# Kernel optimization log

Measured on AMD Instinct MI355X. Metric: run time of the kernel, lower is better.

The kernel has to match this reference:

```python
import jax, jax.numpy as jnp
import numpy as np

N_NODES = 100000

def gcn_conv(x, edge_index, W, b):
    # GCNConv with normalize=True and self-loops:
    # out = D^{-1/2} (A + I) D^{-1/2} (x W) + b
    h = x @ W                                   # [N, out]
    src, dst = edge_index[0], edge_index[1]
    deg = jax.ops.segment_sum(jnp.ones(src.shape[0], h.dtype), dst,
                              num_segments=N_NODES) + 1.0  # +1 for self loop
    dinv = jax.lax.rsqrt(deg)
    norm = dinv[src] * dinv[dst]                # [E]
    agg = jax.ops.segment_sum(h[src] * norm[:, None], dst,
                              num_segments=N_NODES)        # [N, out]
    agg = agg + h * (1.0 / deg)[:, None]        # self-loop term: norm_ii = 1/deg_i
    return agg + b


def setup_inputs() -> dict:
    key = jax.random.key(0)
    k0, k1, k2, k3 = jax.random.split(key, 4)
    N, E, F_IN, H, C = N_NODES, 1600000, 256, 128, 40
    x = jax.random.normal(k0, (N, F_IN), dtype=jnp.float32)
    edge_index = jax.random.randint(k1, (2, E), 0, N, dtype=jnp.int64)
    W1 = jax.random.normal(k2, (F_IN, H), dtype=jnp.float32) * (1.0 / np.sqrt(F_IN))
    b1 = jnp.zeros((H,), jnp.float32)
    W2 = jax.random.normal(k3, (H, C), dtype=jnp.float32) * (1.0 / np.sqrt(H))
    b2 = jnp.zeros((C,), jnp.float32)
    return {"x": x, "edge_index": edge_index, "W1": W1, "b1": b1, "W2": W2, "b2": b2}


def reference(x, edge_index, W1, b1, W2, b2):
    # layer 1 + ReLU (dropout = identity in eval mode)
    h = jax.nn.relu(gcn_conv(x, edge_index, W1, b1))
    # final layer (no activation)
    return gcn_conv(h, edge_index, W2, b2)
```

## Files before the change

kernel.cpp:

```cpp
#include <hip/hip_runtime.h>
#include <hip/hip_bf16.h>


#define FIN 256
#define HDIM 128
#define CDIM 40
#define CAP 8192
#define EC 8192

typedef __attribute__((ext_vector_type(8))) short bf16x8;
typedef __attribute__((ext_vector_type(4))) float f32x4;
typedef __attribute__((ext_vector_type(2))) float f32x2;

__device__ inline short f2bf(float f) {
    unsigned u = __float_as_uint(f);
    unsigned r = (u + 0x7FFFu + ((u >> 16) & 1u)) >> 16;
    return (short)r;
}
__device__ inline float bflo(unsigned u) { return __uint_as_float(u << 16); }
__device__ inline float bfhi(unsigned u) { return __uint_as_float(u & 0xFFFF0000u); }
__device__ inline f32x2 unpk(unsigned u) { return (f32x2){bflo(u), bfhi(u)}; }
__device__ inline float ub0(unsigned u) { return (float)(u & 255u); }
__device__ inline float ub1(unsigned u) { return (float)((u >> 8) & 255u); }
__device__ inline float ub2(unsigned u) { return (float)((u >> 16) & 255u); }
__device__ inline float ub3(unsigned u) { return (float)(u >> 24); }

__global__ __launch_bounds__(1024) void scatter_k(const int* __restrict__ ei, int* __restrict__ gcnt,
                                                  int* __restrict__ bmem, int E, int NBUCK) {
    __shared__ int hist[512];
    __shared__ int base[512];
    const int tid = threadIdx.x;
    for (int t = tid; t < NBUCK; t += 1024) hist[t] = 0;
    __syncthreads();
    const int e0 = blockIdx.x * EC;
    const int e1 = min(E, e0 + EC);
    for (int e = e0 + tid; e < e1; e += 1024) atomicAdd(&hist[ei[E + e] >> 8], 1);
    __syncthreads();
    for (int t = tid; t < NBUCK; t += 1024) base[t] = atomicAdd(&gcnt[t], hist[t]);
    __syncthreads();
    for (int e = e0 + tid; e < e1; e += 1024) {
        int s = ei[e];
        int d = ei[E + e];
        int b = d >> 8;
        int pos = atomicAdd(&base[b], 1);
        bmem[b * CAP + pos] = s | ((d & 255) << 20);
    }
}

__global__ __launch_bounds__(256) void p2_build_k(const int* __restrict__ bmem, const int* __restrict__ bcnt,
                                                  int* __restrict__ csr, int2* __restrict__ nseg,
                                                  float* __restrict__ dinv, float* __restrict__ invd,
                                                  const float* __restrict__ W1, const float* __restrict__ W2,
                                                  short* __restrict__ W1T, short* __restrict__ W2T, int N) {
    __shared__ int hist[256], cur[256], sc[256];
    __shared__ int stage[CAP];
    const int b = blockIdx.x;
    const int tid = threadIdx.x;

    for (int idx = b * 256 + tid; idx < FIN * HDIM + 48 * HDIM; idx += gridDim.x * 256) {
        if (idx < FIN * HDIM) {
            int k = idx >> 7, n = idx & 127;
            W1T[n * FIN + k] = f2bf(W1[idx]);
        } else {
            int j = idx - FIN * HDIM;
            int c = j >> 7, k = j & 127;
            W2T[j] = (c < CDIM) ? f2bf(W2[k * CDIM + c]) : (short)0;
        }
    }

    int cnt = bcnt[b];
    if (cnt > CAP) cnt = CAP;
    const int* src = bmem + b * CAP;
    hist[tid] = 0;
    __syncthreads();
    for (int j = tid; j < cnt; j += 256) atomicAdd(&hist[src[j] >> 20], 1);
    __syncthreads();
    int v = hist[tid];
    sc[tid] = v;
    __syncthreads();
    for (int off = 1; off < 256; off <<= 1) {
        int t = (tid >= off) ? sc[tid - off] : 0;
        __syncthreads();
        sc[tid] += t;
        __syncthreads();
    }
    int excl = sc[tid] - v;
    cur[tid] = excl;
    int i = b * 256 + tid;
    if (i < N) {
        nseg[i] = make_int2(b * CAP + excl, v);
        float dg = (float)(v + 1);
        dinv[i] = rsqrtf(dg);
        invd[i] = 1.0f / dg;
    }
    __syncthreads();
    for (int j = tid; j < cnt; j += 256) {
        int rec = src[j];
        int pos = atomicAdd(&cur[rec >> 20], 1);
        stage[pos] = rec & 0xFFFFF;
    }
    __syncthreads();
    int* dst = csr + b * CAP;
    for (int j = tid; j < cnt; j += 256) dst[j] = stage[j];
}

#define LDSTRIDE 40
__global__ __launch_bounds__(256) void gemm1_mfma_k(const float* __restrict__ X,
                                                    const short* __restrict__ W1T,
                                                    const float* __restrict__ dinv,
                                                    unsigned char* __restrict__ T1q,
                                                    float* __restrict__ scl,
                                                    float* __restrict__ wsc, int N) {
    __shared__ short SH[128 * LDSTRIDE * 2];
    short* As = SH;
    short* Bs = SH + 128 * LDSTRIDE;
    const int tid = threadIdx.x;
    const int lane = tid & 63;
    const int wid = tid >> 6;
    const int w0 = wid & 1, w1 = wid >> 1;
    const int quad = lane >> 4;
    const int l16 = lane & 15;
    const int rowbase = blockIdx.x * 128;
    const int sr = tid >> 1;
    const int sh = tid & 1;

    f32x4 acc[4][4];
#pragma unroll
    for (int a = 0; a < 4; a++)
#pragma unroll
        for (int b = 0; b < 4; b++) acc[a][b] = (f32x4){0.f, 0.f, 0.f, 0.f};

    const int arow = min(rowbase + sr, N - 1);
    const float* xsrc = X + (size_t)arow * FIN + sh * 16;
    const int4* bsrc = (const int4*)(W1T + (size_t)sr * FIN + sh * 16);

    for (int k0 = 0; k0 < FIN; k0 += 32) {
        float vals[16];
        *(float4*)&vals[0]  = *(const float4*)(xsrc + k0);
        *(float4*)&vals[4]  = *(const float4*)(xsrc + k0 + 4);
        *(float4*)&vals[8]  = *(const float4*)(xsrc + k0 + 8);
        *(float4*)&vals[12] = *(const float4*)(xsrc + k0 + 12);
        short tmp[16];
#pragma unroll
        for (int c = 0; c < 16; c++) tmp[c] = f2bf(vals[c]);
        ((int4*)&As[sr * LDSTRIDE + sh * 16])[0] = ((int4*)tmp)[0];
        ((int4*)&As[sr * LDSTRIDE + sh * 16])[1] = ((int4*)tmp)[1];
        int4 b0 = bsrc[k0 >> 3];
        int4 b1 = bsrc[(k0 >> 3) + 1];
        ((int4*)&Bs[sr * LDSTRIDE + sh * 16])[0] = b0;
        ((int4*)&Bs[sr * LDSTRIDE + sh * 16])[1] = b1;
        __syncthreads();

        bf16x8 afr[4], bfr[4];
#pragma unroll
        for (int mt = 0; mt < 4; mt++)
            afr[mt] = *(const bf16x8*)&As[(w1 * 64 + mt * 16 + l16) * LDSTRIDE + quad * 8];
#pragma unroll
        for (int nt = 0; nt < 4; nt++)
            bfr[nt] = *(const bf16x8*)&Bs[(w0 * 64 + nt * 16 + l16) * LDSTRIDE + quad * 8];
#pragma unroll
        for (int mt = 0; mt < 4; mt++)
#pragma unroll
            for (int nt = 0; nt < 4; nt++)
                acc[mt][nt] = __builtin_amdgcn_mfma_f32_16x16x32_bf16(afr[mt], bfr[nt], acc[mt][nt], 0, 0, 0);
        __syncthreads();
    }

    unsigned char* qbuf = (unsigned char*)SH;
    float* rmaxb = (float*)((char*)SH + 16384);
#pragma unroll
    for (int mt = 0; mt < 4; mt++) {
#pragma unroll
        for (int r = 0; r < 4; r++) {
            float m = fabsf(acc[mt][0][r]);
            m = fmaxf(m, fabsf(acc[mt][1][r]));
            m = fmaxf(m, fabsf(acc[mt][2][r]));
            m = fmaxf(m, fabsf(acc[mt][3][r]));
#pragma unroll
            for (int off = 1; off < 16; off <<= 1) m = fmaxf(m, __shfl_xor(m, off));
            rmaxb[w0 * 128 + w1 * 64 + mt * 16 + quad * 4 + r] = m;
        }
    }
    __syncthreads();
    if (tid < 128) {
        int grow = rowbase + tid;
        if (grow < N) {
            float rv = fmaxf(rmaxb[tid], rmaxb[128 + tid]);
            float s = rv * (1.f / 127.f);
            scl[grow] = s;
            wsc[grow] = s * dinv[grow];
        }
    }
#pragma unroll
    for (int mt = 0; mt < 4; mt++) {
#pragma unroll
        for (int r = 0; r < 4; r++) {
            const int row = w1 * 64 + mt * 16 + quad * 4 + r;
            float rv = fmaxf(rmaxb[row], rmaxb[128 + row]);
            float qinv = rv > 0.f ? 127.f / rv : 0.f;
#pragma unroll
            for (int nt = 0; nt < 4; nt++) {
                int qi = (int)rintf(acc[mt][nt][r] * qinv) + 128;
                qi = qi < 0 ? 0 : (qi > 255 ? 255 : qi);
                qbuf[row * 128 + w0 * 64 + nt * 16 + l16] = (unsigned char)qi;
            }
        }
    }
    __syncthreads();
#pragma unroll
    for (int it = 0; it < 4; it++) {
        int idx = tid + it * 256;
        int row = idx >> 3;
        if (rowbase + row < N)
            ((uint4*)(T1q + (size_t)(rowbase + row) * 128))[idx & 7] = ((const uint4*)qbuf)[idx];
    }
}

__global__ __launch_bounds__(256) void agg1_k(const unsigned char* __restrict__ T1q, const int2* __restrict__ nseg,
                                              const int* __restrict__ csr, const float* __restrict__ wsc,
                                              const float* __restrict__ scl, const float* __restrict__ dinv,
                                              const float* __restrict__ invd, const float* __restrict__ b1,
                                              unsigned* __restrict__ Hb, int N) {
    const int lane = threadIdx.x & 63;
    const int quad = lane >> 4;
    const int ql = lane & 15;
    const int i = blockIdx.x * 4 + (threadIdx.x >> 6);
    if (i >= N) return;
    const int2 sg = nseg[i];
    const int e0 = sg.x, deg = sg.y;
    int sv = 0; float wv = 0.f;
    if (lane < deg) { sv = csr[e0 + lane]; wv = wsc[sv]; }

    const uint2* rowp = (const uint2*)T1q;
    uint2 us = rowp[i * 16 + ql];
    const float sscale = scl[i];

    f32x2 acc[4]; float asum = 0.f;
#pragma unroll
    for (int t = 0; t < 4; t++) acc[t] = (f32x2){0.f, 0.f};

    const int dmain = deg < 64 ? deg : 64;
    for (int j = 0; j < dmain; j += 16) {
        const int i0 = j + quad, i1 = j + 4 + quad, i2 = j + 8 + quad, i3 = j + 12 + quad;
        int s0 = __shfl(sv, i0); int s1 = __shfl(sv, i1);
        int s2 = __shfl(sv, i2); int s3 = __shfl(sv, i3);
        float w0 = __shfl(wv, i0); float w1 = __shfl(wv, i1);
        float w2 = __shfl(wv, i2); float w3 = __shfl(wv, i3);
        w0 = (i0 < dmain) ? w0 : 0.f;
        w1 = (i1 < dmain) ? w1 : 0.f;
        w2 = (i2 < dmain) ? w2 : 0.f;
        w3 = (i3 < dmain) ? w3 : 0.f;
        uint2 u0 = rowp[s0 * 16 + ql];
        uint2 u1 = rowp[s1 * 16 + ql];
        uint2 u2 = rowp[s2 * 16 + ql];
        uint2 u3 = rowp[s3 * 16 + ql];
        asum += w0 + w1 + w2 + w3;
        f32x2 W0 = (f32x2){w0, w0}, W1v = (f32x2){w1, w1}, W2v = (f32x2){w2, w2}, W3v = (f32x2){w3, w3};
        acc[0] += W0 * (f32x2){ub0(u0.x), ub1(u0.x)} + W1v * (f32x2){ub0(u1.x), ub1(u1.x)}
                + W2v * (f32x2){ub0(u2.x), ub1(u2.x)} + W3v * (f32x2){ub0(u3.x), ub1(u3.x)};
        acc[1] += W0 * (f32x2){ub2(u0.x), ub3(u0.x)} + W1v * (f32x2){ub2(u1.x), ub3(u1.x)}
                + W2v * (f32x2){ub2(u2.x), ub3(u2.x)} + W3v * (f32x2){ub2(u3.x), ub3(u3.x)};
        acc[2] += W0 * (f32x2){ub0(u0.y), ub1(u0.y)} + W1v * (f32x2){ub0(u1.y), ub1(u1.y)}
                + W2v * (f32x2){ub0(u2.y), ub1(u2.y)} + W3v * (f32x2){ub0(u3.y), ub1(u3.y)};
        acc[3] += W0 * (f32x2){ub2(u0.y), ub3(u0.y)} + W1v * (f32x2){ub2(u1.y), ub3(u1.y)}
                + W2v * (f32x2){ub2(u2.y), ub3(u2.y)} + W3v * (f32x2){ub2(u3.y), ub3(u3.y)};
    }
    const int eEnd = e0 + deg;
    for (int e = e0 + 64; e < eEnd; e += 4) {
        int idx = e + quad;
        int cl = idx < eEnd ? idx : eEnd - 1;
        int sj = csr[cl];
        float wj = (idx < eEnd) ? wsc[sj] : 0.f;
        uint2 u = rowp[sj * 16 + ql];
        asum += wj;
        f32x2 Wj = (f32x2){wj, wj};
        acc[0] += Wj * (f32x2){ub0(u.x), ub1(u.x)};
        acc[1] += Wj * (f32x2){ub2(u.x), ub3(u.x)};
        acc[2] += Wj * (f32x2){ub0(u.y), ub1(u.y)};
        acc[3] += Wj * (f32x2){ub2(u.y), ub3(u.y)};
    }
#pragma unroll
    for (int t = 0; t < 4; t++) {
        acc[t].x += __shfl_xor(acc[t].x, 16); acc[t].y += __shfl_xor(acc[t].y, 16);
        acc[t].x += __shfl_xor(acc[t].x, 32); acc[t].y += __shfl_xor(acc[t].y, 32);
    }
    asum += __shfl_xor(asum, 16);
    asum += __shfl_xor(asum, 32);

    const float di = dinv[i];
    const float sf2 = invd[i] * sscale;
    const float K = -128.f * (sf2 + di * asum);
    float4 bA = *(const float4*)(b1 + ql * 8);
    float4 bB = *(const float4*)(b1 + ql * 8 + 4);
    float o0 = fmaxf(bA.x + sf2 * ub0(us.x) + di * acc[0].x + K, 0.f);
    float o1 = fmaxf(bA.y + sf2 * ub1(us.x) + di * acc[0].y + K, 0.f);
    float o2 = fmaxf(bA.z + sf2 * ub2(us.x) + di * acc[1].x + K, 0.f);
    float o3 = fmaxf(bA.w + sf2 * ub3(us.x) + di * acc[1].y + K, 0.f);
    float o4 = fmaxf(bB.x + sf2 * ub0(us.y) + di * acc[2].x + K, 0.f);
    float o5 = fmaxf(bB.y + sf2 * ub1(us.y) + di * acc[2].y + K, 0.f);
    float o6 = fmaxf(bB.z + sf2 * ub2(us.y) + di * acc[3].x + K, 0.f);
    float o7 = fmaxf(bB.w + sf2 * ub3(us.y) + di * acc[3].y + K, 0.f);
    uint4 pk;
    pk.x = ((unsigned)(unsigned short)f2bf(o0)) | (((unsigned)(unsigned short)f2bf(o1)) << 16);
    pk.y = ((unsigned)(unsigned short)f2bf(o2)) | (((unsigned)(unsigned short)f2bf(o3)) << 16);
    pk.z = ((unsigned)(unsigned short)f2bf(o4)) | (((unsigned)(unsigned short)f2bf(o5)) << 16);
    pk.w = ((unsigned)(unsigned short)f2bf(o6)) | (((unsigned)(unsigned short)f2bf(o7)) << 16);
    if (quad == 0) ((uint4*)(Hb + (size_t)i * 64))[ql] = pk;
}

__global__ __launch_bounds__(256) void gemm2_mfma_k(const short* __restrict__ Hb,
                                                    const short* __restrict__ W2T,
                                                    short* __restrict__ T2b, int N) {
    __shared__ short As[128 * LDSTRIDE];
    __shared__ short Bs[48 * LDSTRIDE];
    const int tid = threadIdx.x;
    const int lane = tid & 63;
    const int wid = tid >> 6;
    const int quad = lane >> 4;
    const int l16 = lane & 15;
    const int rowbase = blockIdx.x * 128;
    const int sr = tid >> 1;
    const int sh = tid & 1;

    f32x4 acc[2][3];
#pragma unroll
    for (int a = 0; a < 2; a++)
#pragma unroll
        for (int b = 0; b < 3; b++) acc[a][b] = (f32x4){0.f, 0.f, 0.f, 0.f};

    const int arow = min(rowbase + sr, N - 1);
    const int4* asrc = (const int4*)(Hb + (size_t)arow * HDIM + sh * 16);
    const int br = tid >> 1, bh = tid & 1;
    const int4* bsrc = (const int4*)(W2T + br * HDIM + bh * 16);

    for (int k0 = 0; k0 < HDIM; k0 += 32) {
        int4 a0 = asrc[k0 >> 3];
        int4 a1 = asrc[(k0 >> 3) + 1];
        ((int4*)&As[sr * LDSTRIDE + sh * 16])[0] = a0;
        ((int4*)&As[sr * LDSTRIDE + sh * 16])[1] = a1;
        if (tid < 96) {
            int4 b0 = bsrc[k0 >> 3];
            int4 b1 = bsrc[(k0 >> 3) + 1];
            ((int4*)&Bs[br * LDSTRIDE + bh * 16])[0] = b0;
            ((int4*)&Bs[br * LDSTRIDE + bh * 16])[1] = b1;
        }
        __syncthreads();
        bf16x8 afr[2], bfr[3];
#pragma unroll
        for (int mt = 0; mt < 2; mt++)
            afr[mt] = *(const bf16x8*)&As[(wid * 32 + mt * 16 + l16) * LDSTRIDE + quad * 8];
#pragma unroll
        for (int nt = 0; nt < 3; nt++)
            bfr[nt] = *(const bf16x8*)&Bs[(nt * 16 + l16) * LDSTRIDE + quad * 8];
#pragma unroll
        for (int mt = 0; mt < 2; mt++)
#pragma unroll
            for (int nt = 0; nt < 3; nt++)
                acc[mt][nt] = __builtin_amdgcn_mfma_f32_16x16x32_bf16(afr[mt], bfr[nt], acc[mt][nt], 0, 0, 0);
        __syncthreads();
    }
#pragma unroll
    for (int mt = 0; mt < 2; mt++) {
#pragma unroll
        for (int r = 0; r < 4; r++) {
            int row = rowbase + wid * 32 + mt * 16 + quad * 4 + r;
            if (row < N) {
#pragma unroll
                for (int nt = 0; nt < 3; nt++) {
                    int col = nt * 16 + l16;
                    T2b[(size_t)row * 48 + col] = f2bf(acc[mt][nt][r]);
                }
            }
        }
    }
}

__global__ __launch_bounds__(256) void agg2_k(const short* __restrict__ T2b, const int2* __restrict__ nseg,
                                              const int* __restrict__ csr, const float* __restrict__ dinv,
                                              const float* __restrict__ invd, const float* __restrict__ b2,
                                              float* __restrict__ OUT, int N) {
    const int lane = threadIdx.x & 63;
    const int oct = lane >> 3;
    const int olr = lane & 7;
    const int ol = olr < 6 ? olr : 5;
    const bool act = olr < 6;
    const int i = blockIdx.x * 4 + (threadIdx.x >> 6);
    if (i >= N) return;
    const int2 sg = nseg[i];
    const int e0 = sg.x, deg = sg.y;
    int sv = 0; float wv = 0.f;
    if (lane < deg) { sv = csr[e0 + lane]; wv = dinv[sv]; }

    const uint4* rowp = (const uint4*)T2b;
    f32x2 acc[4];
#pragma unroll
    for (int t = 0; t < 4; t++) acc[t] = (f32x2){0.f, 0.f};

    const int dmain = deg < 64 ? deg : 64;
    for (int j = 0; j < dmain; j += 16) {
        const int i0 = j + oct, i1 = j + 8 + oct;
        int s0 = __shfl(sv, i0); int s1 = __shfl(sv, i1);
        float w0 = __shfl(wv, i0); float w1 = __shfl(wv, i1);
        w0 = (i0 < dmain && act) ? w0 : 0.f;
        w1 = (i1 < dmain && act) ? w1 : 0.f;
        uint4 u0 = rowp[s0 * 6 + ol];
        uint4 u1 = rowp[s1 * 6 + ol];
        f32x2 W0 = (f32x2){w0, w0}, W1v = (f32x2){w1, w1};
        acc[0] += W0 * unpk(u0.x) + W1v * unpk(u1.x);
        acc[1] += W0 * unpk(u0.y) + W1v * unpk(u1.y);
        acc[2] += W0 * unpk(u0.z) + W1v * unpk(u1.z);
        acc[3] += W0 * unpk(u0.w) + W1v * unpk(u1.w);
    }
    const int eEnd = e0 + deg;
    for (int e = e0 + 64; e < eEnd; e += 8) {
        int idx = e + oct;
        int cl = idx < eEnd ? idx : eEnd - 1;
        int sj = csr[cl];
        float wj = (idx < eEnd && act) ? dinv[sj] : 0.f;
        uint4 u = rowp[sj * 6 + ol];
        f32x2 Wj = (f32x2){wj, wj};
        acc[0] += Wj * unpk(u.x);
        acc[1] += Wj * unpk(u.y);
        acc[2] += Wj * unpk(u.z);
        acc[3] += Wj * unpk(u.w);
    }
#pragma unroll
    for (int t = 0; t < 4; t++) {
        acc[t].x += __shfl_xor(acc[t].x, 8);  acc[t].y += __shfl_xor(acc[t].y, 8);
        acc[t].x += __shfl_xor(acc[t].x, 16); acc[t].y += __shfl_xor(acc[t].y, 16);
        acc[t].x += __shfl_xor(acc[t].x, 32); acc[t].y += __shfl_xor(acc[t].y, 32);
    }
    if (oct == 0 && olr < 5) {
        const float di = dinv[i], sf = invd[i];
        uint4 us = rowp[i * 6 + olr];
        float4 bA = *(const float4*)(b2 + olr * 8);
        float4 bB = *(const float4*)(b2 + olr * 8 + 4);
        float4 oA, oB;
        oA.x = bA.x + sf * bflo(us.x) + di * acc[0].x;
        oA.y = bA.y + sf * bfhi(us.x) + di * acc[0].y;
        oA.z = bA.z + sf * bflo(us.y) + di * acc[1].x;
        oA.w = bA.w + sf * bfhi(us.y) + di * acc[1].y;
        oB.x = bB.x + sf * bflo(us.z) + di * acc[2].x;
        oB.y = bB.y + sf * bfhi(us.z) + di * acc[2].y;
        oB.z = bB.z + sf * bflo(us.w) + di * acc[3].x;
        oB.w = bB.w + sf * bfhi(us.w) + di * acc[3].y;
        *(float4*)(OUT + (size_t)i * CDIM + olr * 8) = oA;
        *(float4*)(OUT + (size_t)i * CDIM + olr * 8 + 4) = oB;
    }
}

extern "C" void kernel_launch(void* const* d_in, const int* in_sizes, int n_in,
                              void* d_out, int out_size, void* d_ws, size_t ws_size,
                              hipStream_t stream) {
    const float* x   = (const float*)d_in[0];
    const int*   ei  = (const int*)d_in[1];
    const float* W1  = (const float*)d_in[2];
    const float* b1  = (const float*)d_in[3];
    const float* W2  = (const float*)d_in[4];
    const float* b2  = (const float*)d_in[5];
    float*       out = (float*)d_out;

    const int Hd  = in_sizes[3];
    const int Fin = in_sizes[2] / Hd;
    const int N   = in_sizes[0] / Fin;
    const int E   = in_sizes[1] / 2;

    const int NBUCK = (N + 255) / 256;
    const int NB1   = (E + EC - 1) / EC;

    char* base = (char*)d_ws;
    size_t off = 0;
    auto alloc = [&](size_t bytes) -> void* {
        void* p = base + off;
        off += (bytes + 255) & ~(size_t)255;
        return p;
    };
    size_t bmemB = (size_t)NBUCK * CAP * 4;
    size_t t1qB  = (size_t)N * 128;
    size_t regA  = bmemB > t1qB ? bmemB : t1qB;
    char* pA = (char*)alloc(regA);
    int*           bmem = (int*)pA;
    unsigned char* t1q  = (unsigned char*)pA;

    int*      gcnt = (int*)alloc((size_t)NBUCK * 4);
    int*      csr  = (int*)alloc((size_t)NBUCK * CAP * 4);
    int2*     nseg = (int2*)alloc((size_t)N * 8);
    float*    dinv = (float*)alloc((size_t)N * 4);
    float*    invd = (float*)alloc((size_t)N * 4);
    float*    scl  = (float*)alloc((size_t)N * 4);
    float*    wsc  = (float*)alloc((size_t)N * 4);
    short*    W1T  = (short*)alloc((size_t)HDIM * FIN * 2);
    short*    W2T  = (short*)alloc((size_t)48 * HDIM * 2);
    unsigned* hb   = (unsigned*)alloc((size_t)N * HDIM * 2);
    short*    t2b  = (short*)alloc((size_t)N * 48 * 2);

    hipMemsetAsync(gcnt, 0, (size_t)NBUCK * 4, stream);
    scatter_k<<<NB1, 1024, 0, stream>>>(ei, gcnt, bmem, E, NBUCK);
    p2_build_k<<<NBUCK, 256, 0, stream>>>(bmem, gcnt, csr, nseg, dinv, invd, W1, W2, W1T, W2T, N);

    gemm1_mfma_k<<<(N + 127) / 128, 256, 0, stream>>>(x, W1T, dinv, t1q, scl, wsc, N);
    agg1_k<<<(N + 3) / 4, 256, 0, stream>>>(t1q, nseg, csr, wsc, scl, dinv, invd, b1, hb, N);
    gemm2_mfma_k<<<(N + 127) / 128, 256, 0, stream>>>((const short*)hb, W2T, t2b, N);
    agg2_k<<<(N + 3) / 4, 256, 0, stream>>>(t2b, nseg, csr, dinv, invd, b2, out, N);
}
```

Measured before the change: 321.7 us.

## Fuse second GEMM into layer-1 aggregation and quantize layer-2 features to uint8

The layer-1 aggregation kernel now multiplies each node's ReLU output by W2 with per-wave MFMA, using lane shuffles to build the A fragment. It then quantizes the 40-wide result to uint8 with a per-row scale and writes 64-byte rows. This drops the bf16 hidden buffer, the separate gemm2 kernel launch and its global round trip. The second aggregation gathers uint8 rows (64 B instead of 96 B per neighbor) and applies the same zero-point correction used in layer 1. Running the MFMA on a single row per wave leaves most of each tile idle, and 8-bit quantization of the layer-2 features adds rounding error to the output.

```diff
diff --git a/kernel.cpp b/kernel.cpp
--- a/kernel.cpp
+++ b/kernel.cpp
@@ -220,7 +220,10 @@
                                               const int* __restrict__ csr, const float* __restrict__ wsc,
                                               const float* __restrict__ scl, const float* __restrict__ dinv,
                                               const float* __restrict__ invd, const float* __restrict__ b1,
-                                              unsigned* __restrict__ Hb, int N) {
+                                              const short* __restrict__ W2T,
+                                              unsigned char* __restrict__ T2q,
+                                              float* __restrict__ scl2, float* __restrict__ wsc2, int N) {
+    __shared__ unsigned char qs[4][64];
     const int lane = threadIdx.x & 63;
     const int quad = lane >> 4;
     const int ql = lane & 15;
@@ -305,94 +308,67 @@
     pk.y = ((unsigned)(unsigned short)f2bf(o2)) | (((unsigned)(unsigned short)f2bf(o3)) << 16);
     pk.z = ((unsigned)(unsigned short)f2bf(o4)) | (((unsigned)(unsigned short)f2bf(o5)) << 16);
     pk.w = ((unsigned)(unsigned short)f2bf(o6)) | (((unsigned)(unsigned short)f2bf(o7)) << 16);
-    if (quad == 0) ((uint4*)(Hb + (size_t)i * 64))[ql] = pk;
-}
-
-__global__ __launch_bounds__(256) void gemm2_mfma_k(const short* __restrict__ Hb,
-                                                    const short* __restrict__ W2T,
-                                                    short* __restrict__ T2b, int N) {
-    __shared__ short As[128 * LDSTRIDE];
-    __shared__ short Bs[48 * LDSTRIDE];
-    const int tid = threadIdx.x;
-    const int lane = tid & 63;
-    const int wid = tid >> 6;
-    const int quad = lane >> 4;
-    const int l16 = lane & 15;
-    const int rowbase = blockIdx.x * 128;
-    const int sr = tid >> 1;
-    const int sh = tid & 1;
-
-    f32x4 acc[2][3];
-#pragma unroll
-    for (int a = 0; a < 2; a++)
-#pragma unroll
-        for (int b = 0; b < 3; b++) acc[a][b] = (f32x4){0.f, 0.f, 0.f, 0.f};
-
-    const int arow = min(rowbase + sr, N - 1);
-    const int4* asrc = (const int4*)(Hb + (size_t)arow * HDIM + sh * 16);
-    const int br = tid >> 1, bh = tid & 1;
-    const int4* bsrc = (const int4*)(W2T + br * HDIM + bh * 16);
-
-    for (int k0 = 0; k0 < HDIM; k0 += 32) {
-        int4 a0 = asrc[k0 >> 3];
-        int4 a1 = asrc[(k0 >> 3) + 1];
-        ((int4*)&As[sr * LDSTRIDE + sh * 16])[0] = a0;
-        ((int4*)&As[sr * LDSTRIDE + sh * 16])[1] = a1;
-        if (tid < 96) {
-            int4 b0 = bsrc[k0 >> 3];
-            int4 b1 = bsrc[(k0 >> 3) + 1];
-            ((int4*)&Bs[br * LDSTRIDE + bh * 16])[0] = b0;
-            ((int4*)&Bs[br * LDSTRIDE + bh * 16])[1] = b1;
-        }
-        __syncthreads();
-        bf16x8 afr[2], bfr[3];
-#pragma unroll
-        for (int mt = 0; mt < 2; mt++)
-            afr[mt] = *(const bf16x8*)&As[(wid * 32 + mt * 16 + l16) * LDSTRIDE + quad * 8];
+
+    const bf16x8* w2p = (const bf16x8*)W2T;
+    f32x4 acc2[3];
+#pragma unroll
+    for (int nt = 0; nt < 3; nt++) acc2[nt] = (f32x4){0.f, 0.f, 0.f, 0.f};
+#pragma unroll
+    for (int kf = 0; kf < 4; kf++) {
+        const int srcl = kf * 4 + quad;
+        bf16x8 af;
+        ((int*)&af)[0] = __shfl((int)pk.x, srcl);
+        ((int*)&af)[1] = __shfl((int)pk.y, srcl);
+        ((int*)&af)[2] = __shfl((int)pk.z, srcl);
+        ((int*)&af)[3] = __shfl((int)pk.w, srcl);
 #pragma unroll
         for (int nt = 0; nt < 3; nt++)
-            bfr[nt] = *(const bf16x8*)&Bs[(nt * 16 + l16) * LDSTRIDE + quad * 8];
-#pragma unroll
-        for (int mt = 0; mt < 2; mt++)
-#pragma unroll
-            for (int nt = 0; nt < 3; nt++)
-                acc[mt][nt] = __builtin_amdgcn_mfma_f32_16x16x32_bf16(afr[mt], bfr[nt], acc[mt][nt], 0, 0, 0);
-        __syncthreads();
-    }
-#pragma unroll
-    for (int mt = 0; mt < 2; mt++) {
-#pragma unroll
-        for (int r = 0; r < 4; r++) {
-            int row = rowbase + wid * 32 + mt * 16 + quad * 4 + r;
-            if (row < N) {
-#pragma unroll
-                for (int nt = 0; nt < 3; nt++) {
-                    int col = nt * 16 + l16;
-                    T2b[(size_t)row * 48 + col] = f2bf(acc[mt][nt][r]);
-                }
-            }
-        }
-    }
-}
-
-__global__ __launch_bounds__(256) void agg2_k(const short* __restrict__ T2b, const int2* __restrict__ nseg,
-                                              const int* __restrict__ csr, const float* __restrict__ dinv,
+            acc2[nt] = __builtin_amdgcn_mfma_f32_16x16x32_bf16(af, w2p[(nt * 16 + ql) * 16 + srcl], acc2[nt], 0, 0, 0);
+    }
+    float v0 = acc2[0][0];
+    float v1 = acc2[1][0];
+    float v2 = (ql < 8) ? acc2[2][0] : 0.f;
+    float m2 = fmaxf(fmaxf(fabsf(v0), fabsf(v1)), fabsf(v2));
+#pragma unroll
+    for (int off = 1; off < 16; off <<= 1) m2 = fmaxf(m2, __shfl_xor(m2, off));
+    const float scale2 = m2 * (1.f / 127.f);
+    const float qinv2 = m2 > 0.f ? 127.f / m2 : 0.f;
+    const int q0 = (int)rintf(v0 * qinv2) + 128;
+    const int q1 = (int)rintf(v1 * qinv2) + 128;
+    const int q2 = (ql < 8) ? (int)rintf(v2 * qinv2) + 128 : 128;
+    const int wv_ = threadIdx.x >> 6;
+    if (quad == 0) {
+        qs[wv_][ql]      = (unsigned char)q0;
+        qs[wv_][16 + ql] = (unsigned char)q1;
+        qs[wv_][32 + ql] = (unsigned char)q2;
+    } else if (quad == 1) {
+        qs[wv_][48 + ql] = (unsigned char)128;
+    }
+    __builtin_amdgcn_wave_barrier();
+    if (lane < 4) ((uint4*)(T2q + (size_t)i * 64))[lane] = ((const uint4*)qs[wv_])[lane];
+    if (lane == 0) { scl2[i] = scale2; wsc2[i] = scale2 * di; }
+}
+
+__global__ __launch_bounds__(256) void agg2_k(const unsigned char* __restrict__ T2q, const int2* __restrict__ nseg,
+                                              const int* __restrict__ csr, const float* __restrict__ wsc2,
+                                              const float* __restrict__ scl2, const float* __restrict__ dinv,
                                               const float* __restrict__ invd, const float* __restrict__ b2,
                                               float* __restrict__ OUT, int N) {
     const int lane = threadIdx.x & 63;
     const int oct = lane >> 3;
     const int olr = lane & 7;
-    const int ol = olr < 6 ? olr : 5;
-    const bool act = olr < 6;
     const int i = blockIdx.x * 4 + (threadIdx.x >> 6);
     if (i >= N) return;
     const int2 sg = nseg[i];
     const int e0 = sg.x, deg = sg.y;
     int sv = 0; float wv = 0.f;
-    if (lane < deg) { sv = csr[e0 + lane]; wv = dinv[sv]; }
-
-    const uint4* rowp = (const uint4*)T2b;
-    f32x2 acc[4];
+    if (lane < deg) { sv = csr[e0 + lane]; wv = wsc2[sv]; }
+
+    const uint2* rowp = (const uint2*)T2q;
+    uint2 us = rowp[i * 8 + olr];
+    const float sscale = scl2[i];
+
+    f32x2 acc[4]; float asum = 0.f;
 #pragma unroll
     for (int t = 0; t < 4; t++) acc[t] = (f32x2){0.f, 0.f};
 
@@ -401,28 +377,30 @@
         const int i0 = j + oct, i1 = j + 8 + oct;
         int s0 = __shfl(sv, i0); int s1 = __shfl(sv, i1);
         float w0 = __shfl(wv, i0); float w1 = __shfl(wv, i1);
-        w0 = (i0 < dmain && act) ? w0 : 0.f;
-        w1 = (i1 < dmain && act) ? w1 : 0.f;
-        uint4 u0 = rowp[s0 * 6 + ol];
-        uint4 u1 = rowp[s1 * 6 + ol];
+        w0 = (i0 < dmain) ? w0 : 0.f;
+        w1 = (i1 < dmain) ? w1 : 0.f;
+        uint2 u0 = rowp[s0 * 8 + olr];
+        uint2 u1 = rowp[s1 * 8 + olr];
+        asum += w0 + w1;
         f32x2 W0 = (f32x2){w0, w0}, W1v = (f32x2){w1, w1};
-        acc[0] += W0 * unpk(u0.x) + W1v * unpk(u1.x);
-        acc[1] += W0 * unpk(u0.y) + W1v * unpk(u1.y);
-        acc[2] += W0 * unpk(u0.z) + W1v * unpk(u1.z);
-        acc[3] += W0 * unpk(u0.w) + W1v * unpk(u1.w);
+        acc[0] += W0 * (f32x2){ub0(u0.x), ub1(u0.x)} + W1v * (f32x2){ub0(u1.x), ub1(u1.x)};
+        acc[1] += W0 * (f32x2){ub2(u0.x), ub3(u0.x)} + W1v * (f32x2){ub2(u1.x), ub3(u1.x)};
+        acc[2] += W0 * (f32x2){ub0(u0.y), ub1(u0.y)} + W1v * (f32x2){ub0(u1.y), ub1(u1.y)};
+        acc[3] += W0 * (f32x2){ub2(u0.y), ub3(u0.y)} + W1v * (f32x2){ub2(u1.y), ub3(u1.y)};
     }
     const int eEnd = e0 + deg;
     for (int e = e0 + 64; e < eEnd; e += 8) {
         int idx = e + oct;
         int cl = idx < eEnd ? idx : eEnd - 1;
         int sj = csr[cl];
-        float wj = (idx < eEnd && act) ? dinv[sj] : 0.f;
-        uint4 u = rowp[sj * 6 + ol];
+        float wj = (idx < eEnd) ? wsc2[sj] : 0.f;
+        uint2 u = rowp[sj * 8 + olr];
+        asum += wj;
         f32x2 Wj = (f32x2){wj, wj};
-        acc[0] += Wj * unpk(u.x);
-        acc[1] += Wj * unpk(u.y);
-        acc[2] += Wj * unpk(u.z);
-        acc[3] += Wj * unpk(u.w);
+        acc[0] += Wj * (f32x2){ub0(u.x), ub1(u.x)};
+        acc[1] += Wj * (f32x2){ub2(u.x), ub3(u.x)};
+        acc[2] += Wj * (f32x2){ub0(u.y), ub1(u.y)};
+        acc[3] += Wj * (f32x2){ub2(u.y), ub3(u.y)};
     }
 #pragma unroll
     for (int t = 0; t < 4; t++) {
@@ -430,20 +408,25 @@
         acc[t].x += __shfl_xor(acc[t].x, 16); acc[t].y += __shfl_xor(acc[t].y, 16);
         acc[t].x += __shfl_xor(acc[t].x, 32); acc[t].y += __shfl_xor(acc[t].y, 32);
     }
+    asum += __shfl_xor(asum, 8);
+    asum += __shfl_xor(asum, 16);
+    asum += __shfl_xor(asum, 32);
+
     if (oct == 0 && olr < 5) {
-        const float di = dinv[i], sf = invd[i];
-        uint4 us = rowp[i * 6 + olr];
+        const float di = dinv[i];
+        const float sf2 = invd[i] * sscale;
+        const float K = -128.f * (sf2 + di * asum);
         float4 bA = *(const float4*)(b2 + olr * 8);
         float4 bB = *(const float4*)(b2 + olr * 8 + 4);
         float4 oA, oB;
-        oA.x = bA.x + sf * bflo(us.x) + di * acc[0].x;
-        oA.y = bA.y + sf * bfhi(us.x) + di * acc[0].y;
-        oA.z = bA.z + sf * bflo(us.y) + di * acc[1].x;
-        oA.w = bA.w + sf * bfhi(us.y) + di * acc[1].y;
-        oB.x = bB.x + sf * bflo(us.z) + di * acc[2].x;
-        oB.y = bB.y + sf * bfhi(us.z) + di * acc[2].y;
-        oB.z = bB.z + sf * bflo(us.w) + di * acc[3].x;
-        oB.w = bB.w + sf * bfhi(us.w) + di * acc[3].y;
+        oA.x = bA.x + sf2 * ub0(us.x) + di * acc[0].x + K;
+        oA.y = bA.y + sf2 * ub1(us.x) + di * acc[0].y + K;
+        oA.z = bA.z + sf2 * ub2(us.x) + di * acc[1].x + K;
+        oA.w = bA.w + sf2 * ub3(us.x) + di * acc[1].y + K;
+        oB.x = bB.x + sf2 * ub0(us.y) + di * acc[2].x + K;
+        oB.y = bB.y + sf2 * ub1(us.y) + di * acc[2].y + K;
+        oB.z = bB.z + sf2 * ub2(us.y) + di * acc[3].x + K;
+        oB.w = bB.w + sf2 * ub3(us.y) + di * acc[3].y + K;
         *(float4*)(OUT + (size_t)i * CDIM + olr * 8) = oA;
         *(float4*)(OUT + (size_t)i * CDIM + olr * 8 + 4) = oB;
     }
@@ -489,17 +472,17 @@
     float*    invd = (float*)alloc((size_t)N * 4);
     float*    scl  = (float*)alloc((size_t)N * 4);
     float*    wsc  = (float*)alloc((size_t)N * 4);
+    float*    scl2 = (float*)alloc((size_t)N * 4);
+    float*    wsc2 = (float*)alloc((size_t)N * 4);
     short*    W1T  = (short*)alloc((size_t)HDIM * FIN * 2);
     short*    W2T  = (short*)alloc((size_t)48 * HDIM * 2);
-    unsigned* hb   = (unsigned*)alloc((size_t)N * HDIM * 2);
-    short*    t2b  = (short*)alloc((size_t)N * 48 * 2);
+    unsigned char* t2q = (unsigned char*)alloc((size_t)N * 64);
 
     hipMemsetAsync(gcnt, 0, (size_t)NBUCK * 4, stream);
     scatter_k<<<NB1, 1024, 0, stream>>>(ei, gcnt, bmem, E, NBUCK);
     p2_build_k<<<NBUCK, 256, 0, stream>>>(bmem, gcnt, csr, nseg, dinv, invd, W1, W2, W1T, W2T, N);
 
     gemm1_mfma_k<<<(N + 127) / 128, 256, 0, stream>>>(x, W1T, dinv, t1q, scl, wsc, N);
-    agg1_k<<<(N + 3) / 4, 256, 0, stream>>>(t1q, nseg, csr, wsc, scl, dinv, invd, b1, hb, N);
-    gemm2_mfma_k<<<(N + 127) / 128, 256, 0, stream>>>((const short*)hb, W2T, t2b, N);
-    agg2_k<<<(N + 3) / 4, 256, 0, stream>>>(t2b, nseg, csr, dinv, invd, b2, out, N);
-}
+    agg1_k<<<(N + 3) / 4, 256, 0, stream>>>(t1q, nseg, csr, wsc, scl, dinv, invd, b1, W2T, t2q, scl2, wsc2, N);
+    agg2_k<<<(N + 3) / 4, 256, 0, stream>>>(t2q, nseg, csr, wsc2, scl2, dinv, invd, b2, out, N);
+}
```

Result: slower. 431.4 us (+34.1%).
